# Optimization experiments

Measured on AMD Instinct MI355X. Metric: run time of the kernel, lower is better.

## Reference

```python
import jax, jax.numpy as jnp
import numpy as np

jax.config.update("jax_enable_x64", True)

SIGMA = 10            # STDP time window
POPULATIONS = 2
LR = 1e-3
IN_FEATURES = 1568    # populations * 28 * 28
OUT_FEATURES = 10
BATCH = 64
NUM_STEPS = 256
TWO_SIGMA = 2 * SIGMA


def _normalize(LL, prior):
    # clamp to [-7, 0], then log-normalize over population axis / over outputs
    LL = jnp.clip(LL, -7.0, 0.0)
    pf = LL.reshape(POPULATIONS, -1, OUT_FEATURES)
    LL = (pf - jax.nn.logsumexp(pf, axis=0, keepdims=True)).reshape(IN_FEATURES, OUT_FEATURES)
    prior = jnp.clip(prior, -7.0, 0.0)
    prior = prior - jax.nn.logsumexp(prior)
    return LL, prior


def _run(x, LL, prior):
    B, T, F = x.shape
    LL = LL.astype(jnp.float64)
    prior = prior.astype(jnp.float64)
    LL, prior = _normalize(LL, prior)  # __init__ calls normalize_probs()
    # Padded cumulative spike counts: Cp[:, t] = sum_{s < t} x[:, s]
    Cp = jnp.concatenate(
        [jnp.zeros((B, 1, F), jnp.int32), jnp.cumsum(x.astype(jnp.int32), axis=1)], axis=1)
    t = jnp.arange(T)
    lo = jnp.take(Cp, jnp.clip(t - SIGMA + 1, 0, T), axis=1)   # sum_{s <= t-sigma} x, (B,T,F)
    tp_sigma = jnp.take(Cp, t + 1, axis=1) - lo                # LTP trace: spikes in [t-sigma+1, t]
    tp_s2inf = lo                                              # LTD trace: spikes older than sigma
    potential = tp_sigma > 0                                   # OR of binary spikes in sigma-window
    # post_only gate: no presynaptic spike in [t+1-4*sigma, t-1]
    no_pre = (jnp.take(Cp, t, axis=1)
              - jnp.take(Cp, jnp.clip(t + 1 - 4 * SIGMA, 0, T), axis=1)) == 0

    xs = (jnp.moveaxis(x, 1, 0), jnp.moveaxis(potential, 1, 0),
          jnp.moveaxis(tp_sigma, 1, 0), jnp.moveaxis(tp_s2inf, 1, 0),
          jnp.moveaxis(no_pre, 1, 0), t)

    dt = LL.dtype
    ring0 = jnp.zeros((TWO_SIGMA, B, OUT_FEATURES), jnp.int32)
    z0 = jnp.zeros((B, OUT_FEATURES), jnp.int32)
    carry0 = (LL, prior, jnp.asarray(1.0, dt), ring0, z0, z0, jax.random.key(42))

    def step(carry, inp):
        LL, prior, decay, ring, ring_sum, cum, key = carry
        x_t, pot_t, tps_t, tps2_t, nopre_t, tt = inp
        key, sk = jax.random.split(key)
        logits = pot_t.astype(dt) @ LL + prior                  # (B, out)
        w = jax.nn.one_hot(jax.random.categorical(sk, logits, axis=-1),
                           OUT_FEATURES, dtype=dt)              # sampled winners (B, out)
        tpost = ring_sum.astype(dt)                             # post trace, winners in [t-2sig, t-1]
        tpost_inf = (cum - ring_sum).astype(dt)                 # post trace, older than 2*sigma
        ltp = jnp.einsum('bi,bo->io', tps_t.astype(dt), w)
        ltd = jnp.einsum('bi,bo->io', tps2_t.astype(dt), w)
        post_pre = jnp.einsum('bi,bo->io', x_t.astype(dt), tpost)
        post_only = jnp.einsum('bi,bo->io', nopre_t.astype(dt), tpost_inf)
        scale = LR / decay
        LL = LL + ((jnp.exp(-LL) - 1.0) * ltp - ltd - post_pre - post_only) * scale
        ps = w.sum(axis=0)
        prior = prior + ((jnp.exp(-prior) - 1.0) * ps - (1.0 - ps)) * scale
        LL, prior = _normalize(LL, prior)
        wi = w.astype(jnp.int32)
        slot = tt % TWO_SIGMA
        ring_sum = ring_sum + wi - ring[slot]
        ring = ring.at[slot].set(wi)
        cum = cum + wi
        return (LL, prior, decay + 1.0, ring, ring_sum, cum, key), wi

    (LL, prior, *_), winners = jax.lax.scan(step, carry0, xs)
    return winners, LL, prior


def setup_inputs():
    key = jax.random.key(0)
    k1, k2, k3 = jax.random.split(key, 3)
    x = jax.random.randint(k1, (BATCH, NUM_STEPS, IN_FEATURES), 0, 2, dtype=jnp.int32)
    log_likelihood = jax.random.uniform(k2, (IN_FEATURES, OUT_FEATURES), dtype=jnp.float64) * -1.0 - 1.0
    log_prior = jax.random.uniform(k3, (OUT_FEATURES,), dtype=jnp.float64) * -1.0 - 1.0
    return {"x": x, "log_likelihood": log_likelihood, "log_prior": log_prior}


def reference(x, log_likelihood, log_prior):
    winners, _, _ = _run(x, log_likelihood, log_prior)
    return jnp.argmax(winners.sum(axis=0), axis=-1)  # (batch,), as in the torch forward
```

## Files before the change

### kernel.cpp

```cpp
#include <hip/hip_runtime.h>
#include <stdint.h>
#include <math.h>

#define NF 1568
#define PPOP 784
#define NOUT 10
#define NB 64
#define NT 256
#define RINGN 20
#define NBLK 8
#define TPB 512
#define PSH 98
#define TSW 16
#define TCH 64
#define ICH 64
#define LDP 66

__device__ __forceinline__ uint32_t rotl32(uint32_t v, int r){ return (v<<r)|(v>>(32-r)); }

__device__ __forceinline__ void tf2x32(uint32_t k0, uint32_t k1, uint32_t x0, uint32_t x1,
                                       uint32_t& o0, uint32_t& o1){
  uint32_t ks2 = k0 ^ k1 ^ 0x1BD11BDAu;
  x0 += k0; x1 += k1;
#define TF_RND(r) { x0 += x1; x1 = rotl32(x1,(r)); x1 ^= x0; }
  TF_RND(13) TF_RND(15) TF_RND(26) TF_RND(6)
  x0 += k1;  x1 += ks2 + 1u;
  TF_RND(17) TF_RND(29) TF_RND(16) TF_RND(24)
  x0 += ks2; x1 += k0 + 2u;
  TF_RND(13) TF_RND(15) TF_RND(26) TF_RND(6)
  x0 += k0;  x1 += k1 + 3u;
  TF_RND(17) TF_RND(29) TF_RND(16) TF_RND(24)
  x0 += k1;  x1 += ks2 + 4u;
  TF_RND(13) TF_RND(15) TF_RND(26) TF_RND(6)
  x0 += ks2; x1 += k0 + 5u;
#undef TF_RND
  o0 = x0; o1 = x1;
}

__global__ void kInit(const float* __restrict__ prior_in, double* __restrict__ prior,
                      uint32_t* __restrict__ sk){
  int tid = threadIdx.x;
  if (tid == 0){
    uint32_t k0 = 0u, k1 = 42u;
    for (int t = 0; t < NT; t++){
      uint32_t a,b; tf2x32(k0,k1,0u,1u,a,b); sk[2*t] = a; sk[2*t+1] = b;
      uint32_t c,d; tf2x32(k0,k1,0u,0u,c,d); k0 = c; k1 = d;
    }
  }
  if (tid == 1){
    double v[NOUT];
    double m = -1e300;
    for (int o = 0; o < NOUT; o++){
      double p = (double)prior_in[o];
      p = fmin(0.0, fmax(-7.0, p));
      v[o] = p; m = fmax(m, p);
    }
    double s = 0.0;
    for (int o = 0; o < NOUT; o++) s += exp(v[o]-m);
    double lse = log(s) + m;
    for (int o = 0; o < NOUT; o++) prior[o] = v[o] - lse;
  }
}

__global__ void kInitLL(const float* __restrict__ LL_in, double* __restrict__ G){
  int u = blockIdx.x*256 + threadIdx.x;
  int p = u/NOUT, o = u%NOUT;
  if (p >= PPOP) return;
  double l0 = fmin(0.0, fmax(-7.0, (double)LL_in[p*NOUT+o]));
  double l1 = fmin(0.0, fmax(-7.0, (double)LL_in[(p+PPOP)*NOUT+o]));
  double m = fmax(l0,l1);
  double lse = log(exp(l0-m)+exp(l1-m)) + m;
  G[o*NF + p]        = l0 - lse;
  G[o*NF + p + PPOP] = l1 - lse;
}

__global__ void kTraceC(const int* __restrict__ x, uint16_t* __restrict__ stage,
                        uint64_t* __restrict__ hist_st, int* __restrict__ tot_st, int t0){
  int b = blockIdx.y;
  int i = blockIdx.x*256 + threadIdx.x;
  if (i >= NF) return;
  int sidx = b*NF + i;
  uint64_t hist = (t0 == 0) ? 0ull : hist_st[sidx];
  int total     = (t0 == 0) ? 0    : tot_st[sidx];
  const int* xb = x + (size_t)b*NT*NF + i;
  for (int tl = 0; tl < TCH; tl++){
    int t = t0 + tl;
    int xv = xb[(size_t)t*NF];
    hist = (hist << 1) | (uint64_t)(uint32_t)xv;
    total += xv;
    int tps  = __popcll(hist & 0x3FFull);
    int tps2 = total - tps;
    int pot  = (tps > 0) ? 1 : 0;
    int npre = ((hist & 0x000000FFFFFFFFFEull) == 0) ? 1 : 0;
    stage[((size_t)tl*NB + b)*NF + i] =
      (uint16_t)(tps | (tps2<<4) | (pot<<12) | (npre<<13) | (xv<<14));
  }
  hist_st[sidx] = hist; tot_st[sidx] = total;
}

__global__ void kPack(const uint16_t* __restrict__ stage, uint64_t* __restrict__ masks, int t0){
  __shared__ uint16_t ld[NB*LDP];
  int tl = blockIdx.y, chunk = blockIdx.x;
  int i0 = chunk*ICH;
  int tid = threadIdx.x, lane = tid & 63, wv = tid >> 6;
  for (int r = wv; r < NB; r += 4){
    int i = i0 + lane;
    ld[r*LDP + lane] = (i < NF) ? stage[((size_t)tl*NB + r)*NF + i] : (uint16_t)0;
  }
  __syncthreads();
  int t = t0 + tl;
  for (int r = 0; r < 16; r++){
    int il = wv*16 + r;
    int i = i0 + il;
    if (i >= NF) break;
    uint16_t v = ld[lane*LDP + il];
    uint64_t sel = 0;
#pragma unroll
    for (int k = 0; k < 15; k++){
      uint64_t m = __ballot(((v >> k) & 1) != 0);
      if (lane == k) sel = m;
    }
    if (lane < 15) masks[((size_t)t*16 + lane)*NF + i] = sel;
  }
}

__global__ void kGum(const uint32_t* __restrict__ sk, double* __restrict__ gum){
  int t = blockIdx.x;
  uint32_t k0 = sk[2*t], k1 = sk[2*t+1];
  for (int idx = threadIdx.x; idx < NB*NOUT; idx += blockDim.x){
    uint32_t h,l; tf2x32(k0,k1,0u,(uint32_t)idx,h,l);
    uint64_t bits = ((uint64_t)h << 32) | (uint64_t)l;
    uint64_t fb = (bits >> 12) | 0x3FF0000000000000ull;
    double u01 = __longlong_as_double((long long)fb) - 1.0;
    double u = fmax(2.2250738585072014e-308, u01);
    gum[(size_t)t*NB*NOUT + idx] = -log(-log(u));
  }
}

__device__ __forceinline__ uint32_t poll32(uint64_t* addr, uint32_t tag){
  for (;;){
    uint64_t v = __hip_atomic_load(addr, __ATOMIC_RELAXED, __HIP_MEMORY_SCOPE_AGENT);
    if ((uint32_t)(v >> 32) == tag) return (uint32_t)v;
    __builtin_amdgcn_s_sleep(1);
  }
}

__device__ __forceinline__ int shpix(int s, int j){
  return s*PSH + (j < PSH ? j : j + (PPOP - PSH));
}

__global__ void __launch_bounds__(TPB)
kFused(const uint64_t* __restrict__ masks, double* __restrict__ G,
       const double* __restrict__ prior_g, const double* __restrict__ gum,
       uint64_t* part_lo, uint64_t* part_hi, uint64_t* wslots,
       int* __restrict__ out){
  const int bid = blockIdx.x, tid = threadIdx.x;
  const int lane = tid & 63, wv = tid >> 6;

  __shared__ double LL_s[NOUT][NF];
  __shared__ uint64_t scratch[14*196];
  __shared__ double pin_s[NBLK][NOUT];
  __shared__ double red_s[8][NOUT];
  __shared__ double colsum_s[NOUT], shsum_s[NOUT];
  __shared__ double prior_s[NOUT], pv_s[NOUT];
  __shared__ double lse_sh;
  __shared__ uint64_t wm_s[NOUT];
  __shared__ uint64_t ring_s[RINGN*NOUT];
  __shared__ uint64_t TP_s[NOUT][5];
  __shared__ int ring_cnt_s[NB*NOUT];
  __shared__ int cum_s[NB*NOUT];
  __shared__ int wloc_s[8];
  __shared__ uint32_t pk_s[NBLK];
  __shared__ int wlist_s[8][64];

  uint64_t* pot_s = scratch;
  uint64_t* bst   = scratch;

  double* LLf = &LL_s[0][0];
  for (int k = tid; k < NOUT*NF; k += TPB) LLf[k] = G[k];
  if (tid < NOUT) prior_s[tid] = prior_g[tid];
  for (int k = tid; k < RINGN*NOUT; k += TPB) ring_s[k] = 0;
  for (int k = tid; k < NB*NOUT; k += TPB){ ring_cnt_s[k] = 0; cum_s[k] = 0; }
  __syncthreads();

  for (int t = 0; t < NT; t++){
    const uint32_t tag = (uint32_t)(t + 1);
    const int b = bid*8 + wv;
    const uint64_t* M0 = masks + (size_t)t*16*NF;

    if (t == 0){
      double a0=0,a1=0,a2=0,a3=0,a4=0,a5=0,a6=0,a7=0,a8=0,a9=0;
      for (int i = tid; i < NF; i += TPB){
        a0+=LL_s[0][i]; a1+=LL_s[1][i]; a2+=LL_s[2][i]; a3+=LL_s[3][i]; a4+=LL_s[4][i];
        a5+=LL_s[5][i]; a6+=LL_s[6][i]; a7+=LL_s[7][i]; a8+=LL_s[8][i]; a9+=LL_s[9][i];
      }
#define WRED(x) for (int s = 32; s > 0; s >>= 1) x += __shfl_down(x, s, 64);
      WRED(a0) WRED(a1) WRED(a2) WRED(a3) WRED(a4)
      WRED(a5) WRED(a6) WRED(a7) WRED(a8) WRED(a9)
      if (lane == 0){
        red_s[wv][0]=a0; red_s[wv][1]=a1; red_s[wv][2]=a2; red_s[wv][3]=a3;
        red_s[wv][4]=a4; red_s[wv][5]=a5; red_s[wv][6]=a6; red_s[wv][7]=a7;
        red_s[wv][8]=a8; red_s[wv][9]=a9;
      }
      __syncthreads();
      if (tid < NOUT){
        double s = 0.0;
        for (int w8 = 0; w8 < 8; w8++) s += red_s[w8][tid];
        colsum_s[tid] = s;
      }
      __syncthreads();
    } else {
      if (tid < NBLK*NOUT){
        uint32_t lo = poll32(&part_lo[tid], (uint32_t)t);
        uint32_t hi = poll32(&part_hi[tid], (uint32_t)t);
        pin_s[tid/NOUT][tid%NOUT] = __longlong_as_double(((uint64_t)hi << 32) | lo);
      }
      __syncthreads();
      if (t < TSW){
        for (int s = 0; s < NBLK; s++){
          if (s == bid) continue;
          for (int k = tid; k < 2*PSH*NOUT; k += TPB){
            int o = k/(2*PSH), r = k%(2*PSH);
            int i = shpix(s, r);
            LL_s[o][i] = __hip_atomic_load(&G[o*NF + i], __ATOMIC_RELAXED,
                                           __HIP_MEMORY_SCOPE_AGENT);
          }
        }
        __syncthreads();
      }
      if (tid < NOUT){
        double s = 0.0;
        for (int w8 = 0; w8 < NBLK; w8++) s += pin_s[w8][tid];
        colsum_s[tid] = s;
      }
      __syncthreads();
    }

    const uint64_t* potrow = M0 + 12*NF;
    for (int k = tid; k < NF; k += TPB) pot_s[k] = potrow[k];
    __syncthreads();

    {
      double cadd = 0.0;
      if (t < TSW){
        for (int c = 0; c < 25; c++){
          int i = c*64 + lane;
          uint64_t word = (i < NF) ? pot_s[i] : ~0ull;
          uint64_t mm = __ballot(((word >> b) & 1ull) == 0ull);
          while (mm){
            int bb = __ffsll((unsigned long long)mm) - 1; mm &= mm - 1;
            int ii = c*64 + bb;
            if (lane < NOUT) cadd += LL_s[lane][ii];
          }
        }
      } else {
        int cnt = 0;
        for (int c = 0; c < 25; c++){
          int i = c*64 + lane;
          uint64_t word = (i < NF) ? pot_s[i] : ~0ull;
          bool z = ((word >> b) & 1ull) == 0ull;
          uint64_t mm = __ballot(z);
          if (z){
            int pos = __popcll(mm & ((1ull << lane) - 1ull));
            if (cnt + pos < 64) wlist_s[wv][cnt + pos] = i;
          }
          cnt += __popcll(mm);
          if (cnt > 64) break;
        }
        asm volatile("s_waitcnt lgkmcnt(0)" ::: "memory");
        if (cnt <= 64){
          if (lane < NOUT){
            double c0=0, c1=0, c2=0, c3=0;
            int e = 0;
            for (; e + 4 <= cnt; e += 4){
              c0 += __hip_atomic_load(&G[lane*NF + wlist_s[wv][e]],   __ATOMIC_RELAXED, __HIP_MEMORY_SCOPE_AGENT);
              c1 += __hip_atomic_load(&G[lane*NF + wlist_s[wv][e+1]], __ATOMIC_RELAXED, __HIP_MEMORY_SCOPE_AGENT);
              c2 += __hip_atomic_load(&G[lane*NF + wlist_s[wv][e+2]], __ATOMIC_RELAXED, __HIP_MEMORY_SCOPE_AGENT);
              c3 += __hip_atomic_load(&G[lane*NF + wlist_s[wv][e+3]], __ATOMIC_RELAXED, __HIP_MEMORY_SCOPE_AGENT);
            }
            for (; e < cnt; e++)
              c0 += __hip_atomic_load(&G[lane*NF + wlist_s[wv][e]],   __ATOMIC_RELAXED, __HIP_MEMORY_SCOPE_AGENT);
            cadd = ((c0 + c1) + (c2 + c3));
          }
        } else {
          for (int c = 0; c < 25; c++){
            int i = c*64 + lane;
            uint64_t word = (i < NF) ? pot_s[i] : ~0ull;
            uint64_t mm = __ballot(((word >> b) & 1ull) == 0ull);
            while (mm){
              int bb = __ffsll((unsigned long long)mm) - 1; mm &= mm - 1;
              int ii = c*64 + bb;
              if (lane < NOUT)
                cadd += __hip_atomic_load(&G[lane*NF + ii], __ATOMIC_RELAXED,
                                          __HIP_MEMORY_SCOPE_AGENT);
            }
          }
        }
      }
      double v = -1.0e308;
      if (lane < NOUT)
        v = colsum_s[lane] - cadd + prior_s[lane] + gum[((size_t)t*NB + b)*NOUT + lane];
      double best = __shfl(v, 0, 64); int w = 0;
#pragma unroll
      for (int o = 1; o < NOUT; o++){
        double vo = __shfl(v, o, 64);
        if (vo > best){ best = vo; w = o; }
      }
      if (lane == 0) wloc_s[wv] = w;
    }
    __syncthreads();

    if (wv == 0){
      if (lane == 0){
        uint32_t pk = 0;
#pragma unroll
        for (int w8 = 0; w8 < 8; w8++) pk |= ((uint32_t)wloc_s[w8] & 15u) << (w8*4);
        uint64_t* wsl = wslots + (size_t)(t & 1)*NBLK;
        __hip_atomic_store(&wsl[bid], ((uint64_t)tag << 32) | (uint64_t)pk,
                           __ATOMIC_RELAXED, __HIP_MEMORY_SCOPE_AGENT);
      }
      if (lane < NBLK){
        uint64_t* wsl = wslots + (size_t)(t & 1)*NBLK;
        pk_s[lane] = poll32(&wsl[lane], tag);
      }
      int w = (int)((pk_s[lane >> 3] >> ((lane & 7)*4)) & 15u);
#pragma unroll
      for (int o = 0; o < NOUT; o++){
        uint64_t mo = __ballot(w == o);
        if (lane == 0) wm_s[o] = mo;
      }
#pragma unroll
      for (int o = 0; o < NOUT; o++){
        int c = ring_cnt_s[lane*NOUT + o];
#pragma unroll
        for (int pl = 0; pl < 5; pl++){
          uint64_t tp = __ballot(((c >> pl) & 1) != 0);
          if (lane == 0) TP_s[o][pl] = tp;
        }
      }
    } else {
      int st = tid - 64;
      for (int k = st; k < 14*196; k += (TPB - 64)){
        int pl = k / 196, j = k % 196;
        int pid = pl + (pl >= 12 ? 1 : 0);
        bst[pl*196 + j] = M0[(size_t)pid*NF + shpix(bid, j)];
      }
    }
    __syncthreads();

    double scale = 1e-3 / (double)(t + 1);

    for (int u = tid; u < PSH*NOUT; u += TPB){
      int pr = u / NOUT, o = u % NOUT;
      int gp = bid*PSH + pr, gq = gp + PPOP;
      int pj = pr, qj = pr + 98;
      uint64_t wmv = wm_s[o];
      int ltp0 = __popcll(bst[0*196+pj]&wmv) + (__popcll(bst[1*196+pj]&wmv)<<1)
               + (__popcll(bst[2*196+pj]&wmv)<<2) + (__popcll(bst[3*196+pj]&wmv)<<3);
      int ltd0 = __popcll(bst[4*196+pj]&wmv) + (__popcll(bst[5*196+pj]&wmv)<<1)
               + (__popcll(bst[6*196+pj]&wmv)<<2) + (__popcll(bst[7*196+pj]&wmv)<<3)
               + (__popcll(bst[8*196+pj]&wmv)<<4) + (__popcll(bst[9*196+pj]&wmv)<<5)
               + (__popcll(bst[10*196+pj]&wmv)<<6) + (__popcll(bst[11*196+pj]&wmv)<<7);
      int ltp1 = __popcll(bst[0*196+qj]&wmv) + (__popcll(bst[1*196+qj]&wmv)<<1)
               + (__popcll(bst[2*196+qj]&wmv)<<2) + (__popcll(bst[3*196+qj]&wmv)<<3);
      int ltd1 = __popcll(bst[4*196+qj]&wmv) + (__popcll(bst[5*196+qj]&wmv)<<1)
               + (__popcll(bst[6*196+qj]&wmv)<<2) + (__popcll(bst[7*196+qj]&wmv)<<3)
               + (__popcll(bst[8*196+qj]&wmv)<<4) + (__popcll(bst[9*196+qj]&wmv)<<5)
               + (__popcll(bst[10*196+qj]&wmv)<<6) + (__popcll(bst[11*196+qj]&wmv)<<7);
      uint64_t A13 = bst[12*196+pj], A14 = bst[13*196+pj];
      uint64_t B13 = bst[12*196+qj], B14 = bst[13*196+qj];
      int pp0 = 0, pp1 = 0;
#pragma unroll
      for (int pl = 0; pl < 5; pl++){
        uint64_t tp = TP_s[o][pl];
        pp0 += __popcll(A14 & tp) << pl;
        pp1 += __popcll(B14 & tp) << pl;
      }
      int po0 = 0, po1 = 0;
      if (t >= 21 && (A13 | B13)){
        uint64_t mm = A13;
        while (mm){
          int bb = __ffsll((unsigned long long)mm) - 1; mm &= mm - 1;
          po0 += cum_s[bb*NOUT + o] - ring_cnt_s[bb*NOUT + o];
        }
        mm = B13;
        while (mm){
          int bb = __ffsll((unsigned long long)mm) - 1; mm &= mm - 1;
          po1 += cum_s[bb*NOUT + o] - ring_cnt_s[bb*NOUT + o];
        }
      }
      double l0 = LL_s[o][gp], l1 = LL_s[o][gq];
      l0 = l0 + ((exp(-l0)-1.0)*(double)ltp0 - (double)ltd0 - (double)pp0 - (double)po0)*scale;
      l1 = l1 + ((exp(-l1)-1.0)*(double)ltp1 - (double)ltd1 - (double)pp1 - (double)po1)*scale;
      l0 = fmin(0.0, fmax(-7.0, l0));
      l1 = fmin(0.0, fmax(-7.0, l1));
      double m = fmax(l0, l1);
      double lse = log(exp(l0-m)+exp(l1-m)) + m;
      LL_s[o][gp] = l0 - lse;
      LL_s[o][gq] = l1 - lse;
    }
    __syncthreads();

    for (int k = tid; k < 2*PSH*NOUT; k += TPB){
      int o = k/(2*PSH), r = k%(2*PSH);
      int i = shpix(bid, r);
      __hip_atomic_store(&G[o*NF + i], LL_s[o][i], __ATOMIC_RELAXED, __HIP_MEMORY_SCOPE_AGENT);
    }
    {
      double s0=0,s1=0,s2=0,s3=0,s4=0,s5=0,s6=0,s7=0,s8=0,s9=0;
      if (tid < 2*PSH){
        int i = shpix(bid, tid);
        s0=LL_s[0][i]; s1=LL_s[1][i]; s2=LL_s[2][i]; s3=LL_s[3][i]; s4=LL_s[4][i];
        s5=LL_s[5][i]; s6=LL_s[6][i]; s7=LL_s[7][i]; s8=LL_s[8][i]; s9=LL_s[9][i];
      }
      WRED(s0) WRED(s1) WRED(s2) WRED(s3) WRED(s4)
      WRED(s5) WRED(s6) WRED(s7) WRED(s8) WRED(s9)
#undef WRED
      if (lane == 0){
        red_s[wv][0]=s0; red_s[wv][1]=s1; red_s[wv][2]=s2; red_s[wv][3]=s3;
        red_s[wv][4]=s4; red_s[wv][5]=s5; red_s[wv][6]=s6; red_s[wv][7]=s7;
        red_s[wv][8]=s8; red_s[wv][9]=s9;
      }
    }
    asm volatile("s_waitcnt vmcnt(0)" ::: "memory");
    __syncthreads();
    if (tid < NOUT){
      double s = 0.0;
      for (int w8 = 0; w8 < 8; w8++) s += red_s[w8][tid];
      shsum_s[tid] = s;
    }
    __syncthreads();
    if (tid < 2*NOUT){
      int o = tid >> 1, half = tid & 1;
      uint64_t bits = (uint64_t)__double_as_longlong(shsum_s[o]);
      uint32_t w32 = half ? (uint32_t)(bits >> 32) : (uint32_t)bits;
      uint64_t* dst = half ? &part_hi[bid*NOUT + o] : &part_lo[bid*NOUT + o];
      __hip_atomic_store(dst, ((uint64_t)tag << 32) | (uint64_t)w32,
                         __ATOMIC_RELAXED, __HIP_MEMORY_SCOPE_AGENT);
    }

    int slot = t % RINGN;
    for (int k = tid; k < NB*NOUT; k += TPB){
      int bb = k / NOUT, oo = k % NOUT;
      int nbit = (int)((wm_s[oo] >> bb) & 1ull);
      int obit = (int)((ring_s[slot*NOUT + oo] >> bb) & 1ull);
      ring_cnt_s[k] += nbit - obit;
      cum_s[k]      += nbit;
    }
    if (tid < NOUT){
      double ps = (double)__popcll(wm_s[tid]);
      double pr = prior_s[tid];
      pr = pr + ((exp(-pr)-1.0)*ps - (1.0-ps))*scale;
      pr = fmin(0.0, fmax(-7.0, pr));
      pv_s[tid] = pr;
    }
    __syncthreads();
    if (tid < NOUT) ring_s[slot*NOUT + tid] = wm_s[tid];
    if (tid == 0){
      double m = pv_s[0];
      for (int o = 1; o < NOUT; o++) m = fmax(m, pv_s[o]);
      double s = 0.0;
      for (int o = 0; o < NOUT; o++) s += exp(pv_s[o]-m);
      lse_sh = log(s) + m;
    }
    __syncthreads();
    if (tid < NOUT) prior_s[tid] = pv_s[tid] - lse_sh;
    __syncthreads();
  }

  if (bid == 0 && tid < NB){
    int best = cum_s[tid*NOUT]; int w = 0;
    for (int o = 1; o < NOUT; o++){
      int v = cum_s[tid*NOUT + o];
      if (v > best){ best = v; w = o; }
    }
    out[tid] = w;
  }
}

static inline size_t alignup(size_t v){ return (v + 255) & ~(size_t)255; }

extern "C" void kernel_launch(void* const* d_in, const int* in_sizes, int n_in,
                              void* d_out, int out_size, void* d_ws, size_t ws_size,
                              hipStream_t stream){
  (void)in_sizes; (void)n_in; (void)out_size; (void)ws_size;
  const int*   x        = (const int*)d_in[0];
  const float* LL_in    = (const float*)d_in[1];
  const float* prior_in = (const float*)d_in[2];
  int* out = (int*)d_out;

  char* ws = (char*)d_ws;
  size_t off = 0;
  uint64_t* masks   = (uint64_t*)(ws + off); off += alignup((size_t)NT*16*NF*sizeof(uint64_t));
  uint16_t* stage   = (uint16_t*)(ws + off); off += alignup((size_t)TCH*NB*NF*sizeof(uint16_t));
  uint64_t* hist_st = (uint64_t*)(ws + off); off += alignup((size_t)NB*NF*sizeof(uint64_t));
  int*      tot_st  = (int*)(ws + off);      off += alignup((size_t)NB*NF*sizeof(int));
  double*   G       = (double*)(ws + off);   off += alignup((size_t)NOUT*NF*sizeof(double));
  double*   prior   = (double*)(ws + off);   off += alignup(NOUT*sizeof(double));
  uint32_t* sk      = (uint32_t*)(ws + off); off += alignup(NT*2*sizeof(uint32_t));
  double*   gum     = (double*)(ws + off);   off += alignup((size_t)NT*NB*NOUT*sizeof(double));
  uint64_t* part_lo = (uint64_t*)(ws + off); off += alignup((size_t)NBLK*NOUT*sizeof(uint64_t));
  uint64_t* part_hi = (uint64_t*)(ws + off); off += alignup((size_t)NBLK*NOUT*sizeof(uint64_t));
  uint64_t* wslots  = (uint64_t*)(ws + off); off += alignup((size_t)2*NBLK*sizeof(uint64_t));

  kInit<<<1, 256, 0, stream>>>(prior_in, prior, sk);
  kInitLL<<<31, 256, 0, stream>>>(LL_in, G);
  for (int c = 0; c < NT/TCH; c++){
    kTraceC<<<dim3((NF+255)/256, NB), 256, 0, stream>>>(x, stage, hist_st, tot_st, c*TCH);
    kPack<<<dim3((NF+ICH-1)/ICH, TCH), 256, 0, stream>>>(stage, masks, c*TCH);
  }
  kGum<<<NT, 256, 0, stream>>>(sk, gum);

  kFused<<<NBLK, TPB, 0, stream>>>(masks, G, prior, gum, part_lo, part_hi, wslots, out);
}
```

Before: 5.087 ms.

## Overlap per-step loads and updates across thread groups to cut barriers

```diff
diff --git a/kernel.cpp b/kernel.cpp
--- a/kernel.cpp
+++ b/kernel.cpp
@@ -187,6 +187,9 @@
     const uint32_t tag = (uint32_t)(t + 1);
     const int b = bid*8 + wv;
     const uint64_t* M0 = masks + (size_t)t*16*NF;
+    const uint64_t* potrow = M0 + 12*NF;
+
+    double gpre = (lane < NOUT) ? gum[((size_t)t*NB + b)*NOUT + lane] : 0.0;
 
     if (t == 0){
       double a0=0,a1=0,a2=0,a3=0,a4=0,a5=0,a6=0,a7=0,a8=0,a9=0;
@@ -209,13 +212,22 @@
         colsum_s[tid] = s;
       }
       __syncthreads();
+      for (int k = tid; k < NF; k += TPB) pot_s[k] = potrow[k];
+      __syncthreads();
     } else {
       if (tid < NBLK*NOUT){
         uint32_t lo = poll32(&part_lo[tid], (uint32_t)t);
         uint32_t hi = poll32(&part_hi[tid], (uint32_t)t);
         pin_s[tid/NOUT][tid%NOUT] = __longlong_as_double(((uint64_t)hi << 32) | lo);
+      } else if (tid >= 128){
+        for (int k = tid - 128; k < NF; k += (TPB - 128)) pot_s[k] = potrow[k];
       }
       __syncthreads();
+      if (tid < NOUT){
+        double s = 0.0;
+        for (int w8 = 0; w8 < NBLK; w8++) s += pin_s[w8][tid];
+        colsum_s[tid] = s;
+      }
       if (t < TSW){
         for (int s = 0; s < NBLK; s++){
           if (s == bid) continue;
@@ -226,19 +238,9 @@
                                            __HIP_MEMORY_SCOPE_AGENT);
           }
         }
-        __syncthreads();
-      }
-      if (tid < NOUT){
-        double s = 0.0;
-        for (int w8 = 0; w8 < NBLK; w8++) s += pin_s[w8][tid];
-        colsum_s[tid] = s;
       }
       __syncthreads();
     }
-
-    const uint64_t* potrow = M0 + 12*NF;
-    for (int k = tid; k < NF; k += TPB) pot_s[k] = potrow[k];
-    __syncthreads();
 
     {
       double cadd = 0.0;
@@ -299,7 +301,7 @@
       }
       double v = -1.0e308;
       if (lane < NOUT)
-        v = colsum_s[lane] - cadd + prior_s[lane] + gum[((size_t)t*NB + b)*NOUT + lane];
+        v = colsum_s[lane] - cadd + prior_s[lane] + gpre;
       double best = __shfl(v, 0, 64); int w = 0;
 #pragma unroll
       for (int o = 1; o < NOUT; o++){
@@ -401,12 +403,13 @@
     }
     __syncthreads();
 
-    for (int k = tid; k < 2*PSH*NOUT; k += TPB){
-      int o = k/(2*PSH), r = k%(2*PSH);
-      int i = shpix(bid, r);
-      __hip_atomic_store(&G[o*NF + i], LL_s[o][i], __ATOMIC_RELAXED, __HIP_MEMORY_SCOPE_AGENT);
-    }
-    {
+    int slot = t % RINGN;
+    if (tid < 256){
+      for (int k = tid; k < 2*PSH*NOUT; k += 256){
+        int o = k/(2*PSH), r = k%(2*PSH);
+        int i = shpix(bid, r);
+        __hip_atomic_store(&G[o*NF + i], LL_s[o][i], __ATOMIC_RELAXED, __HIP_MEMORY_SCOPE_AGENT);
+      }
       double s0=0,s1=0,s2=0,s3=0,s4=0,s5=0,s6=0,s7=0,s8=0,s9=0;
       if (tid < 2*PSH){
         int i = shpix(bid, tid);
@@ -421,15 +424,42 @@
         red_s[wv][4]=s4; red_s[wv][5]=s5; red_s[wv][6]=s6; red_s[wv][7]=s7;
         red_s[wv][8]=s8; red_s[wv][9]=s9;
       }
-    }
-    asm volatile("s_waitcnt vmcnt(0)" ::: "memory");
+      asm volatile("s_waitcnt vmcnt(0)" ::: "memory");
+    } else {
+      for (int k = tid - 256; k < NB*NOUT; k += 256){
+        int bb = k / NOUT, oo = k % NOUT;
+        int nbit = (int)((wm_s[oo] >> bb) & 1ull);
+        int obit = (int)((ring_s[slot*NOUT + oo] >> bb) & 1ull);
+        ring_cnt_s[k] += nbit - obit;
+        cum_s[k]      += nbit;
+      }
+      if (tid >= 256 && tid < 256 + NOUT){
+        int o = tid - 256;
+        double ps = (double)__popcll(wm_s[o]);
+        double pr = prior_s[o];
+        pr = pr + ((exp(-pr)-1.0)*ps - (1.0-ps))*scale;
+        pr = fmin(0.0, fmax(-7.0, pr));
+        pv_s[o] = pr;
+      }
+    }
     __syncthreads();
+
     if (tid < NOUT){
       double s = 0.0;
-      for (int w8 = 0; w8 < 8; w8++) s += red_s[w8][tid];
+      for (int w8 = 0; w8 < 4; w8++) s += red_s[w8][tid];
       shsum_s[tid] = s;
     }
+    if (tid == 32){
+      double m = pv_s[0];
+      for (int o = 1; o < NOUT; o++) m = fmax(m, pv_s[o]);
+      double s = 0.0;
+      for (int o = 0; o < NOUT; o++) s += exp(pv_s[o]-m);
+      lse_sh = log(s) + m;
+    }
+    if (tid >= 16 && tid < 16 + NOUT)
+      ring_s[slot*NOUT + (tid-16)] = wm_s[tid-16];
     __syncthreads();
+
     if (tid < 2*NOUT){
       int o = tid >> 1, half = tid & 1;
       uint64_t bits = (uint64_t)__double_as_longlong(shsum_s[o]);
@@ -438,33 +468,8 @@
       __hip_atomic_store(dst, ((uint64_t)tag << 32) | (uint64_t)w32,
                          __ATOMIC_RELAXED, __HIP_MEMORY_SCOPE_AGENT);
     }
-
-    int slot = t % RINGN;
-    for (int k = tid; k < NB*NOUT; k += TPB){
-      int bb = k / NOUT, oo = k % NOUT;
-      int nbit = (int)((wm_s[oo] >> bb) & 1ull);
-      int obit = (int)((ring_s[slot*NOUT + oo] >> bb) & 1ull);
-      ring_cnt_s[k] += nbit - obit;
-      cum_s[k]      += nbit;
-    }
-    if (tid < NOUT){
-      double ps = (double)__popcll(wm_s[tid]);
-      double pr = prior_s[tid];
-      pr = pr + ((exp(-pr)-1.0)*ps - (1.0-ps))*scale;
-      pr = fmin(0.0, fmax(-7.0, pr));
-      pv_s[tid] = pr;
-    }
-    __syncthreads();
-    if (tid < NOUT) ring_s[slot*NOUT + tid] = wm_s[tid];
-    if (tid == 0){
-      double m = pv_s[0];
-      for (int o = 1; o < NOUT; o++) m = fmax(m, pv_s[o]);
-      double s = 0.0;
-      for (int o = 0; o < NOUT; o++) s += exp(pv_s[o]-m);
-      lse_sh = log(s) + m;
-    }
-    __syncthreads();
-    if (tid < NOUT) prior_s[tid] = pv_s[tid] - lse_sh;
+    if (tid >= 32 && tid < 32 + NOUT)
+      prior_s[tid-32] = pv_s[tid-32] - lse_sh;
     __syncthreads();
   }
 
```

Result: faster. 4.632 ms (-8.9%).
